# Performance work log

Hardware: AMD Instinct MI355X
Metric: run time of the kernel (lower is better)

## Reference

```python
import jax, jax.numpy as jnp
import numpy as np

N, E, F, H, L, G, C = 100000, 3200000, 128, 64, 3, 128, 2
BN_EPS = 1e-5


def setup_inputs() -> dict:
    key = jax.random.key(0)
    ks = jax.random.split(key, 16)
    def nrm(k, s, sc=0.05):
        return jax.random.normal(k, s, dtype=jnp.float32) * sc
    return {
        "x": jax.random.normal(ks[0], (N, F), dtype=jnp.float32),
        "lin0_W": nrm(ks[1], (F, H)), "lin0_b": nrm(ks[2], (H,)),
        "eps": jnp.zeros((L,), jnp.float32),                      # GINConv eps per layer
        "W1": nrm(ks[3], (L, H, 2 * H)), "b1": nrm(ks[4], (L, 2 * H)),
        "g1": jnp.ones((L, 2 * H), jnp.float32), "be1": jnp.zeros((L, 2 * H), jnp.float32),
        "W2": nrm(ks[5], (L, 2 * H, H)), "b2": nrm(ks[6], (L, H)),
        "gbn": jnp.ones((L - 1, H), jnp.float32), "bbn": jnp.zeros((L - 1, H), jnp.float32),
        "gate_W": nrm(ks[7], (H, 1)), "gate_b": nrm(ks[8], (1,)),
        "pred_W": nrm(ks[9], (H, H)), "pred_b": nrm(ks[10], (H,)),
        "cls_W": nrm(ks[11], (H, C)), "cls_b": nrm(ks[12], (C,)),
        "edge_index": jax.random.randint(ks[13], (2, E), 0, N),
        "batch": jnp.sort(jax.random.randint(ks[14], (N,), 0, G)),
        "num_graphs": G,
    }


def batchnorm(h, gamma, beta):
    # training-mode BN over node axis, biased variance (torch semantics)
    mu = h.mean(axis=0)
    var = h.var(axis=0)
    return gamma * (h - mu) * jax.lax.rsqrt(var + BN_EPS) + beta


def gin_conv(h, src, dst, eps, W1, b1, g1, be1, W2, b2):
    # message = relu(x_j), aggr='add' at destination
    agg = jax.ops.segment_sum(jax.nn.relu(h[src]), dst, num_segments=h.shape[0])
    z = (1.0 + eps) * h + agg
    z = batchnorm(z @ W1 + b1, g1, be1)          # [N, 2H]
    return jax.nn.relu(z) @ W2 + b2              # [N, H]


def reference(x, lin0_W, lin0_b, eps, W1, b1, g1, be1, W2, b2,
              gbn, bbn, gate_W, gate_b, pred_W, pred_b, cls_W, cls_b,
              edge_index, batch, num_graphs):
    src, dst = edge_index[0], edge_index[1]
    h = x @ lin0_W + lin0_b                      # lin0
    h = gin_conv(h, src, dst, eps[0], W1[0], b1[0], g1[0], be1[0], W2[0], b2[0])
    for i in range(1, L):                        # convs + external BN (not after conv1)
        h = gin_conv(h, src, dst, eps[i], W1[i], b1[i], g1[i], be1[i], W2[i], b2[i])
        h = batchnorm(h, gbn[i - 1], bbn[i - 1])
    # attentional aggregation: segment softmax over gate, weighted sum per graph
    gate = h @ gate_W + gate_b                   # [N, 1]
    gmax = jax.ops.segment_max(gate, batch, num_segments=num_graphs)
    w = jnp.exp(gate - gmax[batch])
    wsum = jax.ops.segment_sum(w, batch, num_segments=num_graphs)
    alpha = w / wsum[batch]                      # [N, 1]
    pooled = jax.ops.segment_sum(alpha * h, batch, num_segments=num_graphs)  # [G, H]
    z = jax.nn.relu(pooled @ pred_W + pred_b)
    return z @ cls_W + cls_b                     # [G, C]
```

## Files before the change

### kernel.cpp

```cpp
#include <hip/hip_runtime.h>
#include <hip/hip_bf16.h>

#define NN 100000
#define EE 3200000
#define HH 64
#define H2 128
#define LL 3
#define GG 128
#define BN_EPSF 1e-5f

#define NBUK 782
#define NBLKC 800
#define CHUNK 4000
#define DMAX 5120

static __device__ __forceinline__ float waveReduceSum64(float v){
  #pragma unroll
  for (int off = 32; off > 0; off >>= 1) v += __shfl_xor(v, off, 64);
  return v;
}

static __device__ __forceinline__ unsigned bf16rne(float f){
  unsigned u = __float_as_uint(f);
  return (u + 0x7FFFu + ((u >> 16) & 1u)) >> 16;
}

static __device__ __forceinline__ void acc16(float* z, uint4 A, uint4 B){
  z[0]  += __uint_as_float(A.x << 16); z[1]  += __uint_as_float(A.x & 0xFFFF0000u);
  z[2]  += __uint_as_float(A.y << 16); z[3]  += __uint_as_float(A.y & 0xFFFF0000u);
  z[4]  += __uint_as_float(A.z << 16); z[5]  += __uint_as_float(A.z & 0xFFFF0000u);
  z[6]  += __uint_as_float(A.w << 16); z[7]  += __uint_as_float(A.w & 0xFFFF0000u);
  z[8]  += __uint_as_float(B.x << 16); z[9]  += __uint_as_float(B.x & 0xFFFF0000u);
  z[10] += __uint_as_float(B.y << 16); z[11] += __uint_as_float(B.y & 0xFFFF0000u);
  z[12] += __uint_as_float(B.z << 16); z[13] += __uint_as_float(B.z & 0xFFFF0000u);
  z[14] += __uint_as_float(B.w << 16); z[15] += __uint_as_float(B.w & 0xFFFF0000u);
}

__global__ __launch_bounds__(256) void kA(const int* __restrict__ dst, int* __restrict__ cntmat){
  __shared__ int hist[NBUK];
  int t = threadIdx.x, blk = blockIdx.x;
  for (int j = t; j < NBUK; j += 256) hist[j] = 0;
  __syncthreads();
  const int4* d4 = (const int4*)(dst + blk * CHUNK);
  for (int i = t; i < CHUNK / 4; i += 256){
    int4 d = d4[i];
    atomicAdd(&hist[d.x >> 7], 1);
    atomicAdd(&hist[d.y >> 7], 1);
    atomicAdd(&hist[d.z >> 7], 1);
    atomicAdd(&hist[d.w >> 7], 1);
  }
  __syncthreads();
  for (int j = t; j < NBUK; j += 256) cntmat[j * NBLKC + blk] = hist[j];
}

__global__ __launch_bounds__(1024) void kB1(int* __restrict__ cntmat, int* __restrict__ btotal){
  __shared__ int s[1024];
  int t = threadIdx.x, j = blockIdx.x;
  int v = (t < NBLKC) ? cntmat[j * NBLKC + t] : 0;
  s[t] = v; __syncthreads();
  for (int off = 1; off < 1024; off <<= 1){
    int x = (t >= off) ? s[t - off] : 0; __syncthreads();
    s[t] += x; __syncthreads();
  }
  if (t < NBLKC) cntmat[j * NBLKC + t] = s[t] - v;
  if (t == 1023) btotal[j] = s[t];
}

__global__ __launch_bounds__(1024) void kB2(const int* __restrict__ btotal,
                                            int* __restrict__ bucket_start,
                                            int* __restrict__ row_start){
  __shared__ int s[1024];
  int t = threadIdx.x;
  int v = (t < NBUK) ? btotal[t] : 0;
  s[t] = v; __syncthreads();
  for (int off = 1; off < 1024; off <<= 1){
    int x = (t >= off) ? s[t - off] : 0; __syncthreads();
    s[t] += x; __syncthreads();
  }
  if (t < NBUK) bucket_start[t] = s[t] - v;
  if (t == 0){ bucket_start[NBUK] = EE; row_start[NN] = EE; }
}

__global__ __launch_bounds__(256) void kC(const int* __restrict__ src, const int* __restrict__ dst,
                                          const int* __restrict__ cntmat,
                                          const int* __restrict__ bucket_start,
                                          int* __restrict__ epart){
  __shared__ int off_s[NBUK];
  __shared__ int cur_s[NBUK];
  int t = threadIdx.x, blk = blockIdx.x;
  for (int j = t; j < NBUK; j += 256){
    off_s[j] = bucket_start[j] + cntmat[j * NBLKC + blk];
    cur_s[j] = 0;
  }
  __syncthreads();
  const int4* s4 = (const int4*)(src + blk * CHUNK);
  const int4* d4 = (const int4*)(dst + blk * CHUNK);
  for (int i = t; i < CHUNK / 4; i += 256){
    int4 s = s4[i];
    int4 d = d4[i];
    int j0 = d.x >> 7, j1 = d.y >> 7, j2 = d.z >> 7, j3 = d.w >> 7;
    int l0 = atomicAdd(&cur_s[j0], 1);
    epart[off_s[j0] + l0] = s.x | ((d.x & 127) << 17);
    int l1 = atomicAdd(&cur_s[j1], 1);
    epart[off_s[j1] + l1] = s.y | ((d.y & 127) << 17);
    int l2 = atomicAdd(&cur_s[j2], 1);
    epart[off_s[j2] + l2] = s.z | ((d.z & 127) << 17);
    int l3 = atomicAdd(&cur_s[j3], 1);
    epart[off_s[j3] + l3] = s.w | ((d.w & 127) << 17);
  }
}

__global__ __launch_bounds__(256) void kD(const int* __restrict__ epart,
                                          const int* __restrict__ bucket_start,
                                          int* __restrict__ row_start, int* __restrict__ elist){
  __shared__ int src_s[DMAX];
  __shared__ short dloc_s[DMAX];
  __shared__ int elist_s[DMAX];
  __shared__ int cnts[128];
  __shared__ int scan_s[128];
  int t = threadIdx.x, b = blockIdx.x;
  int bb = bucket_start[b], be = bucket_start[b + 1];
  int cnt = be - bb;
  int node_base = b << 7;
  if (t < 128) cnts[t] = 0;
  __syncthreads();
  for (int i = t; i < cnt; i += 256){
    int p = epart[bb + i];
    src_s[i] = p & 0x1FFFF;
    int dl = p >> 17;
    dloc_s[i] = (short)dl;
    atomicAdd(&cnts[dl], 1);
  }
  __syncthreads();
  if (t < 128) scan_s[t] = cnts[t];
  __syncthreads();
  for (int off = 1; off < 128; off <<= 1){
    int x = 0;
    if (t < 128 && t >= off) x = scan_s[t - off];
    __syncthreads();
    if (t < 128) scan_s[t] += x;
    __syncthreads();
  }
  if (t < 128){
    int e = scan_s[t] - cnts[t];
    int node = node_base + t;
    if (node < NN) row_start[node] = bb + e;
    cnts[t] = e;
  }
  __syncthreads();
  for (int i = t; i < cnt; i += 256){
    int pos = atomicAdd(&cnts[(int)dloc_s[i]], 1);
    elist_s[pos] = src_s[i];
  }
  __syncthreads();
  for (int i = t; i < cnt; i += 256) elist[bb + i] = elist_s[i];
}

__global__ __launch_bounds__(256, 4) void k_gemm1(const float* __restrict__ h,
                                                  const unsigned short* __restrict__ hb,
                                                  const int* __restrict__ row_start,
                                                  const int* __restrict__ elist,
                                                  const float* __restrict__ W1,
                                                  const float* __restrict__ b1,
                                                  const float* __restrict__ epsArr,
                                                  int layer,
                                                  unsigned short* __restrict__ y1b,
                                                  double* __restrict__ stats){
  alignas(16) __shared__ float Zs[64 * 64];
  __shared__ float redS[128];
  __shared__ float redQ[128];
  int t = threadIdx.x;
  int R0 = blockIdx.x * 64;
  float epsv = 1.0f + epsArr[layer];
  {
    int r  = t >> 2;
    int kq = (t & 3) * 16;
    int R  = R0 + r;
    float zacc[16];
    if (R < NN){
      const float4* hr = (const float4*)&h[(long long)R * 64 + kq];
      #pragma unroll
      for (int i = 0; i < 4; ++i){
        float4 v = hr[i];
        zacc[4*i+0] = epsv * v.x; zacc[4*i+1] = epsv * v.y;
        zacc[4*i+2] = epsv * v.z; zacc[4*i+3] = epsv * v.w;
      }
      int beg = row_start[R], end = row_start[R + 1];
      int j = beg;
      for (; j + 7 < end; j += 8){
        int s0 = elist[j],   s1 = elist[j+1], s2 = elist[j+2], s3 = elist[j+3];
        int s4 = elist[j+4], s5 = elist[j+5], s6 = elist[j+6], s7 = elist[j+7];
        const uint4* q0 = (const uint4*)(hb + (size_t)s0 * 64 + kq);
        const uint4* q1 = (const uint4*)(hb + (size_t)s1 * 64 + kq);
        const uint4* q2 = (const uint4*)(hb + (size_t)s2 * 64 + kq);
        const uint4* q3 = (const uint4*)(hb + (size_t)s3 * 64 + kq);
        const uint4* q4 = (const uint4*)(hb + (size_t)s4 * 64 + kq);
        const uint4* q5 = (const uint4*)(hb + (size_t)s5 * 64 + kq);
        const uint4* q6 = (const uint4*)(hb + (size_t)s6 * 64 + kq);
        const uint4* q7 = (const uint4*)(hb + (size_t)s7 * 64 + kq);
        uint4 A0 = q0[0], B0 = q0[1];
        uint4 A1 = q1[0], B1 = q1[1];
        uint4 A2 = q2[0], B2 = q2[1];
        uint4 A3 = q3[0], B3 = q3[1];
        uint4 A4 = q4[0], B4 = q4[1];
        uint4 A5 = q5[0], B5 = q5[1];
        uint4 A6 = q6[0], B6 = q6[1];
        uint4 A7 = q7[0], B7 = q7[1];
        acc16(zacc, A0, B0); acc16(zacc, A1, B1);
        acc16(zacc, A2, B2); acc16(zacc, A3, B3);
        acc16(zacc, A4, B4); acc16(zacc, A5, B5);
        acc16(zacc, A6, B6); acc16(zacc, A7, B7);
      }
      for (; j < end; ++j){
        int s0 = elist[j];
        const uint4* q0 = (const uint4*)(hb + (size_t)s0 * 64 + kq);
        acc16(zacc, q0[0], q0[1]);
      }
    } else {
      #pragma unroll
      for (int i = 0; i < 16; ++i) zacc[i] = 0.f;
    }
    #pragma unroll
    for (int i = 0; i < 16; ++i) Zs[r * 64 + kq + i] = zacc[i];
  }
  __syncthreads();
  int c = t & 31, rg = t >> 5;
  int r0 = rg * 8;
  float a0[8], a1[8], a2[8], a3[8];
  #pragma unroll
  for (int r = 0; r < 8; ++r){ a0[r]=0.f; a1[r]=0.f; a2[r]=0.f; a3[r]=0.f; }
  for (int k4 = 0; k4 < 16; ++k4){
    float w0[4], w1[4], w2[4], w3[4];
    #pragma unroll
    for (int kk = 0; kk < 4; ++kk){
      int k = k4 * 4 + kk;
      w0[kk] = W1[k*128 + c];
      w1[kk] = W1[k*128 + c + 32];
      w2[kk] = W1[k*128 + c + 64];
      w3[kk] = W1[k*128 + c + 96];
    }
    #pragma unroll
    for (int r = 0; r < 8; ++r){
      float4 zv = *(const float4*)&Zs[(r0 + r) * 64 + k4 * 4];
      a0[r] += zv.x*w0[0] + zv.y*w0[1] + zv.z*w0[2] + zv.w*w0[3];
      a1[r] += zv.x*w1[0] + zv.y*w1[1] + zv.z*w1[2] + zv.w*w1[3];
      a2[r] += zv.x*w2[0] + zv.y*w2[1] + zv.z*w2[2] + zv.w*w2[3];
      a3[r] += zv.x*w3[0] + zv.y*w3[1] + zv.z*w3[2] + zv.w*w3[3];
    }
  }
  float b0 = b1[c], bb1 = b1[c+32], bb2 = b1[c+64], bb3 = b1[c+96];
  float s0=0,s1=0,s2=0,s3=0,q0=0,q1=0,q2=0,q3=0;
  #pragma unroll
  for (int r = 0; r < 8; ++r){
    int R = R0 + r0 + r;
    if (R < NN){
      float y0 = a0[r] + b0, yA = a1[r] + bb1, yB = a2[r] + bb2, yC = a3[r] + bb3;
      size_t base = (size_t)R * 128;
      y1b[base + c]      = (unsigned short)bf16rne(y0);
      y1b[base + c + 32] = (unsigned short)bf16rne(yA);
      y1b[base + c + 64] = (unsigned short)bf16rne(yB);
      y1b[base + c + 96] = (unsigned short)bf16rne(yC);
      s0 += y0; q0 += y0*y0; s1 += yA; q1 += yA*yA;
      s2 += yB; q2 += yB*yB; s3 += yC; q3 += yC*yC;
    }
  }
  __syncthreads();
  if (t < 128){ redS[t] = 0.f; redQ[t] = 0.f; }
  __syncthreads();
  atomicAdd(&redS[c],      s0); atomicAdd(&redQ[c],      q0);
  atomicAdd(&redS[c + 32], s1); atomicAdd(&redQ[c + 32], q1);
  atomicAdd(&redS[c + 64], s2); atomicAdd(&redQ[c + 64], q2);
  atomicAdd(&redS[c + 96], s3); atomicAdd(&redQ[c + 96], q3);
  __syncthreads();
  if (t < 128){
    atomicAdd(&stats[t],       (double)redS[t]);
    atomicAdd(&stats[128 + t], (double)redQ[t]);
  }
}

__global__ __launch_bounds__(256, 4) void k_gemm_k128(const void* __restrict__ inRaw,
                                                      const float* __restrict__ W,
                                                      const float* __restrict__ b,
                                                      const float* __restrict__ bnp,
                                                      float* __restrict__ out,
                                                      unsigned short* __restrict__ hb,
                                                      double* __restrict__ stats,
                                                      int mode){
  alignas(16) __shared__ float As[64 * 128];
  __shared__ float redS[64];
  __shared__ float redQ[64];
  int t = threadIdx.x;
  int R0 = blockIdx.x * 64;
  {
    #pragma unroll
    for (int i = 0; i < 8; ++i){
      int idx = t + i * 256;
      int r = idx >> 5;
      int kk = idx & 31;
      int R = R0 + r;
      float4 v = make_float4(0.f, 0.f, 0.f, 0.f);
      if (R < NN){
        if (mode & 4){
          uint2 u = ((const uint2*)inRaw)[(size_t)R * 32 + kk];
          v.x = __uint_as_float(u.x << 16);
          v.y = __uint_as_float(u.x & 0xFFFF0000u);
          v.z = __uint_as_float(u.y << 16);
          v.w = __uint_as_float(u.y & 0xFFFF0000u);
        } else {
          v = ((const float4*)inRaw)[(size_t)R * 32 + kk];
        }
        if (mode & 1){
          int k = kk * 4;
          v.x = fmaxf(v.x * bnp[k]   + bnp[128 + k],     0.f);
          v.y = fmaxf(v.y * bnp[k+1] + bnp[128 + k + 1], 0.f);
          v.z = fmaxf(v.z * bnp[k+2] + bnp[128 + k + 2], 0.f);
          v.w = fmaxf(v.w * bnp[k+3] + bnp[128 + k + 3], 0.f);
        }
      }
      *(float4*)&As[idx * 4] = v;
    }
  }
  __syncthreads();
  int c = t & 31, rg = t >> 5;
  int r0 = rg * 8;
  float a0[8], a1[8];
  #pragma unroll
  for (int r = 0; r < 8; ++r){ a0[r]=0.f; a1[r]=0.f; }
  for (int k4 = 0; k4 < 32; ++k4){
    float w0[4], w1[4];
    #pragma unroll
    for (int kk = 0; kk < 4; ++kk){
      int k = k4 * 4 + kk;
      w0[kk] = W[k*64 + c];
      w1[kk] = W[k*64 + c + 32];
    }
    #pragma unroll
    for (int r = 0; r < 8; ++r){
      float4 a = *(const float4*)&As[(r0 + r) * 128 + k4 * 4];
      a0[r] += a.x*w0[0] + a.y*w0[1] + a.z*w0[2] + a.w*w0[3];
      a1[r] += a.x*w1[0] + a.y*w1[1] + a.z*w1[2] + a.w*w1[3];
    }
  }
  float b0 = b[c], bA = b[c + 32];
  float s0=0,s1=0,q0=0,q1=0;
  #pragma unroll
  for (int r = 0; r < 8; ++r){
    int R = R0 + r0 + r;
    if (R < NN){
      float y0 = a0[r] + b0, yA = a1[r] + bA;
      long long base = (long long)R * 64;
      out[base + c] = y0;
      out[base + c + 32] = yA;
      hb[base + c]      = (unsigned short)bf16rne(fmaxf(y0, 0.f));
      hb[base + c + 32] = (unsigned short)bf16rne(fmaxf(yA, 0.f));
      s0 += y0; q0 += y0*y0; s1 += yA; q1 += yA*yA;
    }
  }
  if (mode & 2){
    __syncthreads();
    if (t < 64){ redS[t] = 0.f; redQ[t] = 0.f; }
    __syncthreads();
    atomicAdd(&redS[c], s0);      atomicAdd(&redQ[c], q0);
    atomicAdd(&redS[c + 32], s1); atomicAdd(&redQ[c + 32], q1);
    __syncthreads();
    if (t < 64){
      atomicAdd(&stats[t],      (double)redS[t]);
      atomicAdd(&stats[64 + t], (double)redQ[t]);
    }
  }
}

__global__ void k_bnfin(const double* __restrict__ stats, const float* __restrict__ gamma,
                        const float* __restrict__ beta, float* __restrict__ bnp, int C){
  int t = threadIdx.x;
  if (t < C){
    double s = stats[t], q = stats[C + t];
    double mu = s / (double)NN;
    double var = q / (double)NN - mu * mu;
    float rstd = rsqrtf((float)var + BN_EPSF);
    float sc = gamma[t] * rstd;
    bnp[t] = sc;
    bnp[C + t] = beta[t] - (float)mu * sc;
  }
}

__global__ __launch_bounds__(256) void k_affine(float* __restrict__ h, unsigned short* __restrict__ hb,
                                                const float* __restrict__ bnp){
  int i = blockIdx.x * 256 + threadIdx.x;
  float4* h4 = (float4*)h;
  float4 v = h4[i];
  int base = (i * 4) & 63;
  v.x = v.x * bnp[base + 0] + bnp[64 + base + 0];
  v.y = v.y * bnp[base + 1] + bnp[64 + base + 1];
  v.z = v.z * bnp[base + 2] + bnp[64 + base + 2];
  v.w = v.w * bnp[base + 3] + bnp[64 + base + 3];
  h4[i] = v;
  unsigned w0 = bf16rne(fmaxf(v.x, 0.f)) | (bf16rne(fmaxf(v.y, 0.f)) << 16);
  unsigned w1 = bf16rne(fmaxf(v.z, 0.f)) | (bf16rne(fmaxf(v.w, 0.f)) << 16);
  int row = i >> 4;
  *(uint2*)(hb + (size_t)row * 64 + base) = make_uint2(w0, w1);
}

__global__ __launch_bounds__(256) void k_gate(const float* __restrict__ h, const float* __restrict__ gateW,
                                              const float* __restrict__ gateB, const int* __restrict__ batch,
                                              float* __restrict__ gate, unsigned* __restrict__ gmaxkey){
  int lane = threadIdx.x & 63;
  int wid = blockIdx.x * 4 + (threadIdx.x >> 6);
  int nwaves = gridDim.x * 4;
  int chunk = (NN + nwaves - 1) / nwaves;
  int n0 = wid * chunk;
  int n1 = n0 + chunk; if (n1 > NN) n1 = NN;
  if (n0 >= NN) return;
  float gw = gateW[lane];
  float gb = gateB[0];
  int gcur = batch[n0];
  float mcur = -3.402823466e+38f;
  for (int n = n0; n < n1; ++n){
    int g = batch[n];
    if (g != gcur){
      if (lane == 0){
        unsigned u = __float_as_uint(mcur);
        u = (u & 0x80000000u) ? ~u : (u | 0x80000000u);
        atomicMax(&gmaxkey[gcur], u);
      }
      gcur = g;
      mcur = -3.402823466e+38f;
    }
    float v = h[(long long)n * 64 + lane] * gw;
    v = waveReduceSum64(v) + gb;
    if (lane == 0) gate[n] = v;
    mcur = fmaxf(mcur, v);
  }
  if (lane == 0){
    unsigned u = __float_as_uint(mcur);
    u = (u & 0x80000000u) ? ~u : (u | 0x80000000u);
    atomicMax(&gmaxkey[gcur], u);
  }
}

__global__ __launch_bounds__(256) void k_pool(const float* __restrict__ h, const float* __restrict__ gate,
                                              const int* __restrict__ batch, const unsigned* __restrict__ gmaxkey,
                                              float* __restrict__ wsum, float* __restrict__ pooled){
  int lane = threadIdx.x & 63;
  int wid = blockIdx.x * 4 + (threadIdx.x >> 6);
  int nwaves = gridDim.x * 4;
  int chunk = (NN + nwaves - 1) / nwaves;
  int n0 = wid * chunk;
  int n1 = n0 + chunk; if (n1 > NN) n1 = NN;
  if (n0 >= NN) return;
  int gcur = batch[n0];
  unsigned u = gmaxkey[gcur];
  unsigned bits = (u & 0x80000000u) ? (u ^ 0x80000000u) : ~u;
  float m = __uint_as_float(bits);
  float acc = 0.f, wl = 0.f;
  for (int n = n0; n < n1; ++n){
    int g = batch[n];
    if (g != gcur){
      atomicAdd(&pooled[gcur * 64 + lane], acc);
      if (lane == 0) atomicAdd(&wsum[gcur], wl);
      gcur = g;
      u = gmaxkey[g];
      bits = (u & 0x80000000u) ? (u ^ 0x80000000u) : ~u;
      m = __uint_as_float(bits);
      acc = 0.f; wl = 0.f;
    }
    float w = expf(gate[n] - m);
    acc += w * h[(long long)n * 64 + lane];
    wl += w;
  }
  atomicAdd(&pooled[gcur * 64 + lane], acc);
  if (lane == 0) atomicAdd(&wsum[gcur], wl);
}

__global__ __launch_bounds__(64) void k_head(const float* __restrict__ pooled, const float* __restrict__ wsum,
                                             const float* __restrict__ predW, const float* __restrict__ predB,
                                             const float* __restrict__ clsW, const float* __restrict__ clsB,
                                             float* __restrict__ out){
  int g = blockIdx.x, lane = threadIdx.x;
  __shared__ float p[64];
  p[lane] = pooled[g * 64 + lane] / wsum[g];
  __syncthreads();
  float acc = predB[lane];
  for (int i = 0; i < 64; ++i) acc += p[i] * predW[i * 64 + lane];
  float z = fmaxf(acc, 0.f);
  float c0 = z * clsW[lane * 2 + 0];
  float c1 = z * clsW[lane * 2 + 1];
  c0 = waveReduceSum64(c0);
  c1 = waveReduceSum64(c1);
  if (lane == 0){
    out[g * 2 + 0] = c0 + clsB[0];
    out[g * 2 + 1] = c1 + clsB[1];
  }
}

extern "C" void kernel_launch(void* const* d_in, const int* in_sizes, int n_in,
                              void* d_out, int out_size, void* d_ws, size_t ws_size,
                              hipStream_t stream){
  const float* x     = (const float*)d_in[0];
  const float* lin0W = (const float*)d_in[1];
  const float* lin0b = (const float*)d_in[2];
  const float* eps   = (const float*)d_in[3];
  const float* W1    = (const float*)d_in[4];
  const float* b1    = (const float*)d_in[5];
  const float* g1    = (const float*)d_in[6];
  const float* be1   = (const float*)d_in[7];
  const float* W2    = (const float*)d_in[8];
  const float* b2    = (const float*)d_in[9];
  const float* gbn   = (const float*)d_in[10];
  const float* bbn   = (const float*)d_in[11];
  const float* gateW = (const float*)d_in[12];
  const float* gateB = (const float*)d_in[13];
  const float* predW = (const float*)d_in[14];
  const float* predB = (const float*)d_in[15];
  const float* clsW  = (const float*)d_in[16];
  const float* clsB  = (const float*)d_in[17];
  const int* eidx    = (const int*)d_in[18];
  const int* batch   = (const int*)d_in[19];
  const int* src = eidx;
  const int* dst = eidx + EE;
  float* out = (float*)d_out;

  char* ws = (char*)d_ws;
  size_t off = 0;
  auto alloc = [&](size_t bytes) -> char* {
    char* p = ws + off;
    off += (bytes + 15) & ~(size_t)15;
    return p;
  };
  float* h       = (float*)alloc((size_t)NN * 64 * 4);
  unsigned short* y1b = (unsigned short*)alloc((size_t)NN * 128 * 2);
  int* elist     = (int*)alloc((size_t)EE * 4);
  unsigned short* hb = (unsigned short*)alloc((size_t)NN * 64 * 2);
  int* row_start = (int*)alloc((size_t)(NN + 1) * 4);
  float* gate    = (float*)alloc((size_t)NN * 4);
  double* stats1 = (double*)alloc(256 * 8);
  double* stats2 = (double*)alloc(128 * 8);
  float* bnp1    = (float*)alloc(256 * 4);
  float* bnp2    = (float*)alloc(128 * 4);
  unsigned* gmaxkey = (unsigned*)alloc(128 * 4);
  float* wsum    = (float*)alloc(128 * 4);
  float* pooled  = (float*)alloc(128 * 64 * 4);

  char* ov = (char*)y1b;
  int*  epart       = (int*)ov;
  int*  cntmat      = (int*)(ov + (size_t)EE * 4);
  int*  btotal      = (int*)(ov + (size_t)EE * 4 + (size_t)NBUK * NBLKC * 4);
  int*  bucket_start= (int*)(ov + (size_t)EE * 4 + (size_t)NBUK * NBLKC * 4 + 3136);

  const int GBLK = (NN + 63) / 64;

  kA <<<NBLKC, 256, 0, stream>>>(dst, cntmat);
  kB1<<<NBUK, 1024, 0, stream>>>(cntmat, btotal);
  kB2<<<1, 1024, 0, stream>>>(btotal, bucket_start, row_start);
  kC <<<NBLKC, 256, 0, stream>>>(src, dst, cntmat, bucket_start, epart);
  kD <<<NBUK, 256, 0, stream>>>(epart, bucket_start, row_start, elist);

  k_gemm_k128<<<GBLK, 256, 0, stream>>>(x, lin0W, lin0b, bnp1, h, hb, stats2, 0);

  for (int l = 0; l < LL; ++l){
    hipMemsetAsync(stats1, 0, 256 * 8, stream);
    k_gemm1<<<GBLK, 256, 0, stream>>>(h, hb, row_start, elist, W1 + (size_t)l * 64 * 128,
                                      b1 + l * 128, eps, l, y1b, stats1);
    k_bnfin<<<1, 128, 0, stream>>>(stats1, g1 + l * 128, be1 + l * 128, bnp1, 128);
    if (l > 0) hipMemsetAsync(stats2, 0, 128 * 8, stream);
    int mode = 1 | 4 | (l > 0 ? 2 : 0);
    k_gemm_k128<<<GBLK, 256, 0, stream>>>(y1b, W2 + (size_t)l * 128 * 64, b2 + l * 64,
                                          bnp1, h, hb, stats2, mode);
    if (l > 0){
      k_bnfin<<<1, 64, 0, stream>>>(stats2, gbn + (l - 1) * 64, bbn + (l - 1) * 64, bnp2, 64);
      k_affine<<<(NN * 64 / 4) / 256, 256, 0, stream>>>(h, hb, bnp2);
    }
  }

  hipMemsetAsync(gmaxkey, 0, 128 * 4, stream);
  hipMemsetAsync(wsum, 0, 128 * 4, stream);
  hipMemsetAsync(pooled, 0, 128 * 64 * 4, stream);
  k_gate<<<1024, 256, 0, stream>>>(h, gateW, gateB, batch, gate, gmaxkey);
  k_pool<<<1024, 256, 0, stream>>>(h, gate, batch, gmaxkey, wsum, pooled);
  k_head<<<128, 64, 0, stream>>>(pooled, wsum, predW, predB, clsW, clsB, out);
}
```

Baseline: 884.5 us.

## Fold final batchnorm into pooling, sort rows by degree in aggregation

The last layer's external batchnorm affine pass is removed. Its per-channel scale and shift are instead applied on the fly in the gate and pool kernels, and the bf16 copy of h is no longer written when later layers do not need it. The neighbour-aggregation kernel now sorts its 64 rows by in-degree within each block so that threads in a wave do similar amounts of gather work. The gather unroll is reduced from 8 to 4, which may lower memory-level parallelism in exchange for fewer registers.

```diff
diff --git a/kernel.cpp b/kernel.cpp
--- a/kernel.cpp
+++ b/kernel.cpp
@@ -169,11 +169,29 @@
   alignas(16) __shared__ float Zs[64 * 64];
   __shared__ float redS[128];
   __shared__ float redQ[128];
+  __shared__ int degS[64];
+  __shared__ int permS[64];
   int t = threadIdx.x;
   int R0 = blockIdx.x * 64;
   float epsv = 1.0f + epsArr[layer];
+  if (t < 64){
+    int R = R0 + t;
+    degS[t] = (R < NN) ? (row_start[R + 1] - row_start[R]) : 0;
+  }
+  __syncthreads();
+  if (t < 64){
+    int d = degS[t];
+    int rank = 0;
+    #pragma unroll 8
+    for (int r2 = 0; r2 < 64; ++r2){
+      int d2 = degS[r2];
+      rank += (d2 < d) || (d2 == d && r2 < t);
+    }
+    permS[rank] = t;
+  }
+  __syncthreads();
   {
-    int r  = t >> 2;
+    int r  = permS[t >> 2];
     int kq = (t & 3) * 16;
     int R  = R0 + r;
     float zacc[16];
@@ -187,29 +205,18 @@
       }
       int beg = row_start[R], end = row_start[R + 1];
       int j = beg;
-      for (; j + 7 < end; j += 8){
-        int s0 = elist[j],   s1 = elist[j+1], s2 = elist[j+2], s3 = elist[j+3];
-        int s4 = elist[j+4], s5 = elist[j+5], s6 = elist[j+6], s7 = elist[j+7];
+      for (; j + 3 < end; j += 4){
+        int s0 = elist[j], s1 = elist[j+1], s2 = elist[j+2], s3 = elist[j+3];
         const uint4* q0 = (const uint4*)(hb + (size_t)s0 * 64 + kq);
         const uint4* q1 = (const uint4*)(hb + (size_t)s1 * 64 + kq);
         const uint4* q2 = (const uint4*)(hb + (size_t)s2 * 64 + kq);
         const uint4* q3 = (const uint4*)(hb + (size_t)s3 * 64 + kq);
-        const uint4* q4 = (const uint4*)(hb + (size_t)s4 * 64 + kq);
-        const uint4* q5 = (const uint4*)(hb + (size_t)s5 * 64 + kq);
-        const uint4* q6 = (const uint4*)(hb + (size_t)s6 * 64 + kq);
-        const uint4* q7 = (const uint4*)(hb + (size_t)s7 * 64 + kq);
         uint4 A0 = q0[0], B0 = q0[1];
         uint4 A1 = q1[0], B1 = q1[1];
         uint4 A2 = q2[0], B2 = q2[1];
         uint4 A3 = q3[0], B3 = q3[1];
-        uint4 A4 = q4[0], B4 = q4[1];
-        uint4 A5 = q5[0], B5 = q5[1];
-        uint4 A6 = q6[0], B6 = q6[1];
-        uint4 A7 = q7[0], B7 = q7[1];
         acc16(zacc, A0, B0); acc16(zacc, A1, B1);
         acc16(zacc, A2, B2); acc16(zacc, A3, B3);
-        acc16(zacc, A4, B4); acc16(zacc, A5, B5);
-        acc16(zacc, A6, B6); acc16(zacc, A7, B7);
       }
       for (; j < end; ++j){
         int s0 = elist[j];
@@ -351,8 +358,10 @@
       long long base = (long long)R * 64;
       out[base + c] = y0;
       out[base + c + 32] = yA;
-      hb[base + c]      = (unsigned short)bf16rne(fmaxf(y0, 0.f));
-      hb[base + c + 32] = (unsigned short)bf16rne(fmaxf(yA, 0.f));
+      if (!(mode & 8)){
+        hb[base + c]      = (unsigned short)bf16rne(fmaxf(y0, 0.f));
+        hb[base + c + 32] = (unsigned short)bf16rne(fmaxf(yA, 0.f));
+      }
       s0 += y0; q0 += y0*y0; s1 += yA; q1 += yA*yA;
     }
   }
@@ -403,7 +412,8 @@
 
 __global__ __launch_bounds__(256) void k_gate(const float* __restrict__ h, const float* __restrict__ gateW,
                                               const float* __restrict__ gateB, const int* __restrict__ batch,
-                                              float* __restrict__ gate, unsigned* __restrict__ gmaxkey){
+                                              float* __restrict__ gate, unsigned* __restrict__ gmaxkey,
+                                              const float* __restrict__ bnp){
   int lane = threadIdx.x & 63;
   int wid = blockIdx.x * 4 + (threadIdx.x >> 6);
   int nwaves = gridDim.x * 4;
@@ -411,6 +421,7 @@
   int n0 = wid * chunk;
   int n1 = n0 + chunk; if (n1 > NN) n1 = NN;
   if (n0 >= NN) return;
+  float sc = bnp[lane], sh = bnp[64 + lane];
   float gw = gateW[lane];
   float gb = gateB[0];
   int gcur = batch[n0];
@@ -426,7 +437,8 @@
       gcur = g;
       mcur = -3.402823466e+38f;
     }
-    float v = h[(long long)n * 64 + lane] * gw;
+    float hv = h[(long long)n * 64 + lane] * sc + sh;
+    float v = hv * gw;
     v = waveReduceSum64(v) + gb;
     if (lane == 0) gate[n] = v;
     mcur = fmaxf(mcur, v);
@@ -440,7 +452,8 @@
 
 __global__ __launch_bounds__(256) void k_pool(const float* __restrict__ h, const float* __restrict__ gate,
                                               const int* __restrict__ batch, const unsigned* __restrict__ gmaxkey,
-                                              float* __restrict__ wsum, float* __restrict__ pooled){
+                                              float* __restrict__ wsum, float* __restrict__ pooled,
+                                              const float* __restrict__ bnp){
   int lane = threadIdx.x & 63;
   int wid = blockIdx.x * 4 + (threadIdx.x >> 6);
   int nwaves = gridDim.x * 4;
@@ -448,6 +461,7 @@
   int n0 = wid * chunk;
   int n1 = n0 + chunk; if (n1 > NN) n1 = NN;
   if (n0 >= NN) return;
+  float sc = bnp[lane], sh = bnp[64 + lane];
   int gcur = batch[n0];
   unsigned u = gmaxkey[gcur];
   unsigned bits = (u & 0x80000000u) ? (u ^ 0x80000000u) : ~u;
@@ -465,7 +479,8 @@
       acc = 0.f; wl = 0.f;
     }
     float w = expf(gate[n] - m);
-    acc += w * h[(long long)n * 64 + lane];
+    float hv = h[(long long)n * 64 + lane] * sc + sh;
+    acc += w * hv;
     wl += w;
   }
   atomicAdd(&pooled[gcur * 64 + lane], acc);
@@ -563,19 +578,20 @@
                                       b1 + l * 128, eps, l, y1b, stats1);
     k_bnfin<<<1, 128, 0, stream>>>(stats1, g1 + l * 128, be1 + l * 128, bnp1, 128);
     if (l > 0) hipMemsetAsync(stats2, 0, 128 * 8, stream);
-    int mode = 1 | 4 | (l > 0 ? 2 : 0);
+    int mode = 1 | 4 | (l > 0 ? 2 : 0) | (l >= 1 ? 8 : 0);
     k_gemm_k128<<<GBLK, 256, 0, stream>>>(y1b, W2 + (size_t)l * 128 * 64, b2 + l * 64,
                                           bnp1, h, hb, stats2, mode);
     if (l > 0){
       k_bnfin<<<1, 64, 0, stream>>>(stats2, gbn + (l - 1) * 64, bbn + (l - 1) * 64, bnp2, 64);
-      k_affine<<<(NN * 64 / 4) / 256, 256, 0, stream>>>(h, hb, bnp2);
+      if (l < LL - 1)
+        k_affine<<<(NN * 64 / 4) / 256, 256, 0, stream>>>(h, hb, bnp2);
     }
   }
 
   hipMemsetAsync(gmaxkey, 0, 128 * 4, stream);
   hipMemsetAsync(wsum, 0, 128 * 4, stream);
   hipMemsetAsync(pooled, 0, 128 * 64 * 4, stream);
-  k_gate<<<1024, 256, 0, stream>>>(h, gateW, gateB, batch, gate, gmaxkey);
-  k_pool<<<1024, 256, 0, stream>>>(h, gate, batch, gmaxkey, wsum, pooled);
+  k_gate<<<1024, 256, 0, stream>>>(h, gateW, gateB, batch, gate, gmaxkey, bnp2);
+  k_pool<<<1024, 256, 0, stream>>>(h, gate, batch, gmaxkey, wsum, pooled, bnp2);
   k_head<<<128, 64, 0, stream>>>(pooled, wsum, predW, predB, clsW, clsB, out);
 }
```

Result: faster. 859.7 us (-2.8%).
